# Kernel tuning notes

Hardware: AMD Instinct MI355X
Metric: run time of the kernel (lower is better)

The kernel has to match this reference:

```python
import jax, jax.numpy as jnp
import numpy as np

EPS = 1e-5
KH = KW = 3
PAD = 1

def conv3x3(x, w, b=None):
    out = jax.lax.conv_general_dilated(
        x, w, window_strides=(1, 1), padding=((PAD, PAD), (PAD, PAD)),
        dimension_numbers=("NCHW", "OIHW", "NCHW"))
    if b is not None:
        out = out + b[None, :, None, None]
    return out

def batchnorm(x, gamma, beta):
    # training-mode BatchNorm2d: batch statistics over (N, H, W)
    mean = x.mean(axis=(0, 2, 3), keepdims=True)
    var = x.var(axis=(0, 2, 3), keepdims=True)
    return gamma[None, :, None, None] * (x - mean) / jnp.sqrt(var + EPS) + beta[None, :, None, None]

def bilinear_gather(x, y_pos, x_pos):
    # x: [B,C,H,W]; y_pos/x_pos: [B,P,H,W] (P = KH*KW sampling taps)
    # zero padding outside image (mmcv modulated deform conv semantics)
    B, C, H, W = x.shape
    P = y_pos.shape[1]
    x_flat = x.reshape(B, C, H * W)
    y0 = jnp.floor(y_pos)
    x0 = jnp.floor(x_pos)
    ly = y_pos - y0
    lx = x_pos - x0
    out = jnp.zeros((B, C, P, H, W), dtype=x.dtype)
    for dy, dx, wgt in ((0, 0, (1 - ly) * (1 - lx)), (0, 1, (1 - ly) * lx),
                        (1, 0, ly * (1 - lx)), (1, 1, ly * lx)):
        yi = y0 + dy
        xi = x0 + dx
        valid = ((yi >= 0) & (yi <= H - 1) & (xi >= 0) & (xi <= W - 1)).astype(x.dtype)
        yc = jnp.clip(yi, 0, H - 1).astype(jnp.int32)
        xc = jnp.clip(xi, 0, W - 1).astype(jnp.int32)
        idx = (yc * W + xc).reshape(B, 1, P * H * W)
        vals = jnp.take_along_axis(x_flat, jnp.broadcast_to(idx, (B, C, P * H * W)), axis=2)
        vals = vals.reshape(B, C, P, H, W)
        out = out + vals * (wgt * valid)[:, None]
    return out  # [B,C,P,H,W]

def modulated_deform_conv(x, w_off, b_off, w_dcn):
    B, C, H, W = x.shape
    P = KH * KW
    off = conv3x3(x, w_off, b_off)  # [B, 3*P, H, W]
    o1, o2, m = jnp.split(off, 3, axis=1)
    offset = jnp.concatenate([o1, o2], axis=1)            # [B, 2P, H, W]
    offset = offset.reshape(B, P, 2, H, W)                # channel 2p -> dy, 2p+1 -> dx
    mask = jax.nn.sigmoid(m)                              # [B, P, H, W]
    hh = jnp.arange(H, dtype=x.dtype)
    ww = jnp.arange(W, dtype=x.dtype)
    ky = jnp.arange(KH, dtype=x.dtype)
    kx = jnp.arange(KW, dtype=x.dtype)
    # base sampling grid per tap p = ky*KW + kx: (h - PAD + ky, w - PAD + kx)
    base_y = (hh[None, :] - PAD + ky[:, None])            # [KH, H]
    base_x = (ww[None, :] - PAD + kx[:, None])            # [KW, W]
    base_y = jnp.broadcast_to(base_y[:, None, :, None], (KH, KW, H, W)).reshape(P, H, W)
    base_x = jnp.broadcast_to(base_x[None, :, None, :], (KH, KW, H, W)).reshape(P, H, W)
    y_pos = base_y[None] + offset[:, :, 0]                # [B,P,H,W]
    x_pos = base_x[None] + offset[:, :, 1]
    sampled = bilinear_gather(x, y_pos, x_pos)            # [B,C,P,H,W]
    sampled = sampled * mask[:, None]
    w = w_dcn.reshape(w_dcn.shape[0], C, P)               # [O, C, P]
    return jnp.einsum("bcphw,ocp->bohw", sampled, w)

def setup_inputs() -> dict:
    key = jax.random.key(0)
    ks = jax.random.split(key, 10)
    B, Ch, H, W = 4, 256, 64, 64
    Cin, Cout = 2 * Ch, 256
    P = KH * KW
    inp = {
        "input_v": jax.random.normal(ks[0], (B, Ch, H, W), jnp.float32),
        "input_i": jax.random.normal(ks[1], (B, Ch, H, W), jnp.float32),
        "w_off": jax.random.normal(ks[2], (3 * P, Cin, KH, KW), jnp.float32) * 0.01,
        "b_off": jnp.zeros((3 * P,), jnp.float32),
        "w_dcn": jax.random.normal(ks[3], (Cout, Cin, KH, KW), jnp.float32) * (1.0 / np.sqrt(Cin * P)),
        "gamma1": jnp.ones((Cout,), jnp.float32),
        "beta1": jnp.zeros((Cout,), jnp.float32),
        "w2": jax.random.normal(ks[4], (Cout, Cout, KH, KW), jnp.float32) * (1.0 / np.sqrt(Cout * P)),
        "gamma2": jnp.ones((Cout,), jnp.float32),
        "beta2": jnp.zeros((Cout,), jnp.float32),
    }
    return inp

def reference(input_v, input_i, w_off, b_off, w_dcn, gamma1, beta1, w2, gamma2, beta2):
    x = jnp.concatenate([input_v, input_i], axis=1)
    out = modulated_deform_conv(x, w_off, b_off, w_dcn)
    out = jax.nn.relu(batchnorm(out, gamma1, beta1))
    out = jax.nn.relu(batchnorm(conv3x3(out, w2), gamma2, beta2))
    return out
```

## Files before the change

### kernel.cpp

```cpp
#include <hip/hip_runtime.h>
#include <cstdint>
#include <cstddef>

typedef unsigned short u16;
typedef __attribute__((ext_vector_type(8))) short s16x8;
typedef __attribute__((ext_vector_type(4))) float f32x4;

#define DEV __device__ __forceinline__

DEV float bf2f(short u){
  union { unsigned int i; float f; } v;
  v.i = ((unsigned int)(u16)u) << 16;
  return v.f;
}
DEV short f2bf(float f){
  union { float f; unsigned int i; } v; v.f = f;
  unsigned int u = v.i;
  u += 0x7fffu + ((u >> 16) & 1u);
  return (short)(u >> 16);
}
DEV s16x8 s16x8_zero(){
  s16x8 z;
#pragma unroll
  for(int j=0;j<8;j++) z[j]=0;
  return z;
}
DEV f32x4 f32x4_zero(){
  f32x4 z;
#pragma unroll
  for(int j=0;j<4;j++) z[j]=0.f;
  return z;
}
DEV f32x4 mfma16(s16x8 a, s16x8 b, f32x4 c){
  return __builtin_amdgcn_mfma_f32_16x16x32_bf16(a, b, c, 0, 0, 0);
}

static constexpr size_t OFF_ACC_B  = 0;
static constexpr size_t OUT1_ACC_B = 2097152;
static constexpr size_t OUT2_ACC_B = OUT1_ACC_B + 16777216;
static constexpr size_t STATS_B    = OUT2_ACC_B + 16777216;
static constexpr size_t ZERO_BYTES = STATS_B + 4096;
static constexpr size_t XN_B       = ZERO_BYTES;
static constexpr size_t OUT1N_B    = XN_B + 16777216;
static constexpr size_t WOFFT_B    = OUT1N_B + 8388608;
static constexpr size_t WDCNT_B    = WOFFT_B + 294912;
static constexpr size_t W2T_B      = WDCNT_B + 2359296;

__global__ void k_x_to_nhwc(const float* __restrict__ v, const float* __restrict__ vi,
                            u16* __restrict__ xn){
  __shared__ float tile[64][65];
  const int b = blockIdx.z, c0 = blockIdx.y*64, hw0 = blockIdx.x*64;
  const float* src = (c0 < 256) ? (v  + ((size_t)b*256 + c0)      *4096)
                                : (vi + ((size_t)b*256 + (c0-256))*4096);
  const int t = threadIdx.x;
#pragma unroll
  for(int k=0;k<16;k++){
    int idx = t + k*256;
    int cl = idx >> 6, wl = idx & 63;
    tile[cl][wl] = src[(size_t)cl*4096 + hw0 + wl];
  }
  __syncthreads();
#pragma unroll
  for(int k=0;k<16;k++){
    int idx = t + k*256;
    int wl = idx >> 6, cl = idx & 63;
    xn[(size_t)(b*4096 + hw0 + wl)*512 + c0 + cl] = (u16)f2bf(tile[cl][wl]);
  }
}

__global__ void k_prep_woff(const float* __restrict__ w, u16* __restrict__ wt){
  int idx = blockIdx.x*256 + threadIdx.x;
  if(idx >= 32*4608) return;
  int n = idx / 4608, k = idx % 4608;
  int t = k >> 9, c = k & 511;
  float val = (n < 27) ? w[(size_t)(n*512 + c)*9 + t] : 0.f;
  wt[idx] = (u16)f2bf(val);
}
__global__ void k_prep_wdcn(const float* __restrict__ w, u16* __restrict__ wt){
  int idx = blockIdx.x*256 + threadIdx.x;
  if(idx >= 256*4608) return;
  int n = idx / 4608, k = idx % 4608;
  int t = k >> 9, c = k & 511;
  wt[idx] = (u16)f2bf(w[(size_t)(n*512 + c)*9 + t]);
}
__global__ void k_prep_w2(const float* __restrict__ w, u16* __restrict__ wt){
  int idx = blockIdx.x*256 + threadIdx.x;
  if(idx >= 256*2304) return;
  int n = idx / 2304, k = idx % 2304;
  int t = k >> 8, c = k & 255;
  wt[idx] = (u16)f2bf(w[(size_t)(n*256 + c)*9 + t]);
}

__global__ __launch_bounds__(256, 2) void k_conv_off(
    const u16* __restrict__ xn, const u16* __restrict__ wt, float* __restrict__ offa){
  __shared__ short A_lds[4][128][8];
  __shared__ short B_lds[4][32][8];
  const int tid = threadIdx.x;
  const int lane = tid & 63, wid = tid >> 6;
  const int quad = lane >> 4, ln = lane & 15;
  const int m0 = blockIdx.x * 128;
  const int b = m0 >> 12;
  const int h0 = (m0 & 4095) >> 6;
  const int ks = blockIdx.y;
  const int ts0 = (ks==0)?0:(ks==1)?2:(ks==2)?4:6;
  const int ts1 = (ks==0)?2:(ks==1)?4:(ks==2)?6:9;
  const int m_base = wid * 32;
  const int r = tid >> 1, sp = (tid & 1) * 2;
  const int h_r = h0 + (r >> 6), w_r = r & 63;
  const s16x8* Ap = (const s16x8*)A_lds;
  const s16x8* Bp = (const s16x8*)B_lds;
  f32x4 acc[2][2];
#pragma unroll
  for(int mf=0;mf<2;mf++)
#pragma unroll
    for(int nf=0;nf<2;nf++) acc[mf][nf] = f32x4_zero();

  for(int tp=ts0; tp<ts1; tp++){
    const int ty = tp/3, tx = tp - ty*3;
    const int y = h_r - 1 + ty, x = w_r - 1 + tx;
    const bool vld = (y>=0) & (y<64) & (x>=0) & (x<64);
    const u16* src = xn + (long)(b*4096 + y*64 + x)*512 + sp*8;
    const int kbase = tp*512;
    for(int cc=0; cc<16; cc++){
      const int c0 = cc*32;
      s16x8 v0 = s16x8_zero(), v1 = s16x8_zero();
      if(vld){
        v0 = *(const s16x8*)(src + c0);
        v1 = *(const s16x8*)(src + c0 + 8);
      }
      *(s16x8*)(&A_lds[sp][r][0])   = v0;
      *(s16x8*)(&A_lds[sp+1][r][0]) = v1;
      if(tid < 128){
        const int n = tid & 31, s2 = tid >> 5;
        *(s16x8*)(&B_lds[s2][n][0]) =
            *(const s16x8*)(wt + (size_t)n*4608 + kbase + c0 + s2*8);
      }
      __syncthreads();
      s16x8 a0 = Ap[quad*128 + m_base + ln];
      s16x8 a1 = Ap[quad*128 + m_base + 16 + ln];
      s16x8 b0 = Bp[quad*32 + ln];
      s16x8 b1 = Bp[quad*32 + 16 + ln];
      acc[0][0] = mfma16(a0, b0, acc[0][0]);
      acc[0][1] = mfma16(a0, b1, acc[0][1]);
      acc[1][0] = mfma16(a1, b0, acc[1][0]);
      acc[1][1] = mfma16(a1, b1, acc[1][1]);
      __syncthreads();
    }
  }
#pragma unroll
  for(int mf=0;mf<2;mf++)
#pragma unroll
    for(int nf=0;nf<2;nf++){
      const int col = nf*16 + ln;
#pragma unroll
      for(int i=0;i<4;i++){
        const int row = m_base + mf*16 + quad*4 + i;
        unsafeAtomicAdd(offa + (size_t)(m0+row)*32 + col, acc[mf][nf][i]);
      }
    }
}

__global__ __launch_bounds__(256, 2) void k_dcn(
    const u16* __restrict__ xn, const u16* __restrict__ wt,
    const float* __restrict__ offa, const float* __restrict__ boff,
    float* __restrict__ outa){
  __shared__ short A_lds[4][64][8];
  __shared__ short B_lds[4][256][8];
  __shared__ int   p_ofs[4][64];
  __shared__ float p_wgt[4][64];
  const int tid = threadIdx.x;
  const int lane = tid & 63, wid = tid >> 6;
  const int quad = lane >> 4, ln = lane & 15;
  const int m0 = blockIdx.x * 64;
  const int b = m0 >> 12;
  const int h = (m0 & 4095) >> 6;
  const int ts0 = blockIdx.y ? 4 : 0;
  const int ts1 = blockIdx.y ? 9 : 4;
  const int wm = wid >> 1, wn = wid & 1;
  const int m_base = wm*32, n_base = wn*128;
  const int r = tid >> 2, sub = tid & 3;
  const s16x8* Ap = (const s16x8*)A_lds;
  const s16x8* Bp = (const s16x8*)B_lds;
  f32x4 acc[2][8];
#pragma unroll
  for(int mf=0;mf<2;mf++)
#pragma unroll
    for(int nf=0;nf<8;nf++) acc[mf][nf] = f32x4_zero();

  for(int tp=ts0; tp<ts1; tp++){
    if(tid < 64){
      const int rr = tid;
      const float* orow = offa + (size_t)(m0+rr)*32;
      float dy = orow[2*tp]   + boff[2*tp];
      float dx = orow[2*tp+1] + boff[2*tp+1];
      float mz = orow[18+tp]  + boff[18+tp];
      float mk = 1.f / (1.f + expf(-mz));
      float ypos = (float)(h - 1 + tp/3) + dy;
      float xpos = (float)(rr - 1 + tp%3) + dx;
      float y0f = floorf(ypos), x0f = floorf(xpos);
      float ly = ypos - y0f, lx = xpos - x0f;
      int y0 = (int)y0f, x0 = (int)x0f;
#pragma unroll
      for(int k=0;k<4;k++){
        int ddy = k >> 1, ddx = k & 1;
        int yi = y0 + ddy, xi = x0 + ddx;
        bool vv = (yi >= 0) & (yi < 64) & (xi >= 0) & (xi < 64);
        float wk = (ddy ? ly : 1.f-ly) * (ddx ? lx : 1.f-lx) * mk;
        if(!vv) wk = 0.f;
        int yc = yi < 0 ? 0 : (yi > 63 ? 63 : yi);
        int xc = xi < 0 ? 0 : (xi > 63 ? 63 : xi);
        p_ofs[k][rr] = ((b << 12) + (yc << 6) + xc) << 9;
        p_wgt[k][rr] = wk;
      }
    }
    __syncthreads();
    const float w0f = p_wgt[0][r], w1f = p_wgt[1][r], w2f = p_wgt[2][r], w3f = p_wgt[3][r];
    const u16* s0p = xn + p_ofs[0][r] + sub*8;
    const u16* s1p = xn + p_ofs[1][r] + sub*8;
    const u16* s2p = xn + p_ofs[2][r] + sub*8;
    const u16* s3p = xn + p_ofs[3][r] + sub*8;
    const u16* wrow0 = wt + (size_t)tid*4608 + tp*512;

    for(int cc=0; cc<16; cc++){
      const int c0 = cc*32;
      s16x8 v0 = *(const s16x8*)(s0p + c0);
      s16x8 v1 = *(const s16x8*)(s1p + c0);
      s16x8 v2 = *(const s16x8*)(s2p + c0);
      s16x8 v3 = *(const s16x8*)(s3p + c0);
      s16x8 pk;
#pragma unroll
      for(int j=0;j<8;j++){
        float f = w0f * bf2f(v0[j]);
        f = fmaf(w1f, bf2f(v1[j]), f);
        f = fmaf(w2f, bf2f(v2[j]), f);
        f = fmaf(w3f, bf2f(v3[j]), f);
        pk[j] = f2bf(f);
      }
      *(s16x8*)(&A_lds[sub][r][0]) = pk;
#pragma unroll
      for(int s2=0; s2<4; s2++)
        *(s16x8*)(&B_lds[s2][tid][0]) = *(const s16x8*)(wrow0 + c0 + s2*8);
      __syncthreads();
      s16x8 af0 = Ap[quad*64 + m_base + ln];
      s16x8 af1 = Ap[quad*64 + m_base + 16 + ln];
      s16x8 bfr[8];
#pragma unroll
      for(int nf=0;nf<8;nf++) bfr[nf] = Bp[quad*256 + n_base + nf*16 + ln];
#pragma unroll
      for(int nf=0;nf<8;nf++){
        acc[0][nf] = mfma16(af0, bfr[nf], acc[0][nf]);
        acc[1][nf] = mfma16(af1, bfr[nf], acc[1][nf]);
      }
      __syncthreads();
    }
  }
#pragma unroll
  for(int mf=0;mf<2;mf++)
#pragma unroll
    for(int nf=0;nf<8;nf++){
      const int col = n_base + nf*16 + ln;
#pragma unroll
      for(int i=0;i<4;i++){
        const int row = m_base + mf*16 + quad*4 + i;
        unsafeAtomicAdd(outa + (size_t)(m0+row)*256 + col, acc[mf][nf][i]);
      }
    }
}

__global__ __launch_bounds__(256, 2) void k_conv2(
    const u16* __restrict__ a_in, const u16* __restrict__ wt, float* __restrict__ outa){
  __shared__ short A_lds[4][64][8];
  __shared__ short B_lds[4][256][8];
  const int tid = threadIdx.x;
  const int lane = tid & 63, wid = tid >> 6;
  const int quad = lane >> 4, ln = lane & 15;
  const int m0 = blockIdx.x * 64;
  const int b = m0 >> 12;
  const int h = (m0 & 4095) >> 6;
  const int ts0 = blockIdx.y ? 4 : 0;
  const int ts1 = blockIdx.y ? 9 : 4;
  const int wm = wid >> 1, wn = wid & 1;
  const int m_base = wm*32, n_base = wn*128;
  const int r = tid >> 2, sub = tid & 3;
  const s16x8* Ap = (const s16x8*)A_lds;
  const s16x8* Bp = (const s16x8*)B_lds;
  f32x4 acc[2][8];
#pragma unroll
  for(int mf=0;mf<2;mf++)
#pragma unroll
    for(int nf=0;nf<8;nf++) acc[mf][nf] = f32x4_zero();

  for(int tp=ts0; tp<ts1; tp++){
    const int ty = tp/3, tx = tp - ty*3;
    const int y = h - 1 + ty, x = r - 1 + tx;
    const bool vld = (y>=0) & (y<64) & (x>=0) & (x<64);
    const u16* src = a_in + (long)(b*4096 + y*64 + x)*256 + sub*8;
    const u16* wrow0 = wt + (size_t)tid*2304 + tp*256;
    for(int cc=0; cc<8; cc++){
      const int c0 = cc*32;
      s16x8 va = vld ? *(const s16x8*)(src + c0) : s16x8_zero();
      *(s16x8*)(&A_lds[sub][r][0]) = va;
#pragma unroll
      for(int s2=0;s2<4;s2++)
        *(s16x8*)(&B_lds[s2][tid][0]) = *(const s16x8*)(wrow0 + c0 + s2*8);
      __syncthreads();
      s16x8 af0 = Ap[quad*64 + m_base + ln];
      s16x8 af1 = Ap[quad*64 + m_base + 16 + ln];
      s16x8 bfr[8];
#pragma unroll
      for(int nf=0;nf<8;nf++) bfr[nf] = Bp[quad*256 + n_base + nf*16 + ln];
#pragma unroll
      for(int nf=0;nf<8;nf++){
        acc[0][nf] = mfma16(af0, bfr[nf], acc[0][nf]);
        acc[1][nf] = mfma16(af1, bfr[nf], acc[1][nf]);
      }
      __syncthreads();
    }
  }
#pragma unroll
  for(int mf=0;mf<2;mf++)
#pragma unroll
    for(int nf=0;nf<8;nf++){
      const int col = n_base + nf*16 + ln;
#pragma unroll
      for(int i=0;i<4;i++){
        const int row = m_base + mf*16 + quad*4 + i;
        unsafeAtomicAdd(outa + (size_t)(m0+row)*256 + col, acc[mf][nf][i]);
      }
    }
}

__global__ void k_stats(const float* __restrict__ acc, float* __restrict__ sum,
                        float* __restrict__ sq){
  const int m0 = blockIdx.x*64;
  const int c = threadIdx.x;
  float s = 0.f, q = 0.f;
  for(int i=0;i<64;i++){
    float v = acc[(size_t)(m0+i)*256 + c];
    s += v; q += v*v;
  }
  unsafeAtomicAdd(sum + c, s);
  unsafeAtomicAdd(sq + c, q);
}

__global__ void k_bn1(const float* __restrict__ acc, const float* __restrict__ sum,
                      const float* __restrict__ sq, const float* __restrict__ g,
                      const float* __restrict__ bt, u16* __restrict__ o){
  __shared__ float sc[256], sh[256];
  const int t = threadIdx.x;
  {
    float mean = sum[t] * (1.f/16384.f);
    float var  = sq[t] * (1.f/16384.f) - mean*mean;
    float rstd = rsqrtf(var + 1e-5f);
    float s = g[t] * rstd;
    sc[t] = s; sh[t] = bt[t] - mean*s;
  }
  __syncthreads();
  const int c4 = (t & 63) * 4;
  const float s0 = sc[c4], s1 = sc[c4+1], s2 = sc[c4+2], s3 = sc[c4+3];
  const float h0 = sh[c4], h1 = sh[c4+1], h2 = sh[c4+2], h3 = sh[c4+3];
#pragma unroll
  for(int k=0;k<4;k++){
    int m = blockIdx.x*16 + k*4 + (t>>6);
    const float4 v = *(const float4*)(acc + (size_t)m*256 + c4);
    unsigned int lo = (unsigned int)(u16)f2bf(fmaxf(0.f, v.x*s0 + h0))
                    | ((unsigned int)(u16)f2bf(fmaxf(0.f, v.y*s1 + h1)) << 16);
    unsigned int hi = (unsigned int)(u16)f2bf(fmaxf(0.f, v.z*s2 + h2))
                    | ((unsigned int)(u16)f2bf(fmaxf(0.f, v.w*s3 + h3)) << 16);
    uint2 pr; pr.x = lo; pr.y = hi;
    *(uint2*)(o + (size_t)m*256 + c4) = pr;
  }
}

__global__ void k_bn2_out(const float* __restrict__ acc, const float* __restrict__ sum,
                          const float* __restrict__ sq, const float* __restrict__ g,
                          const float* __restrict__ bt, float* __restrict__ out){
  __shared__ float tile[64][65];
  __shared__ float sc[64], sh[64];
  const int t = threadIdx.x;
  const int b = blockIdx.z, c0 = blockIdx.y*64, hw0 = blockIdx.x*64;
  if(t < 64){
    int c = c0 + t;
    float mean = sum[c] * (1.f/16384.f);
    float var  = sq[c] * (1.f/16384.f) - mean*mean;
    float rstd = rsqrtf(var + 1e-5f);
    float s = g[c] * rstd;
    sc[t] = s; sh[t] = bt[c] - mean*s;
  }
  __syncthreads();
#pragma unroll
  for(int k=0;k<16;k++){
    int idx = t + k*256;
    int wl = idx >> 6, cl = idx & 63;
    float v = acc[(size_t)((b<<12) + hw0 + wl)*256 + c0 + cl];
    tile[wl][cl] = fmaxf(0.f, v*sc[cl] + sh[cl]);
  }
  __syncthreads();
#pragma unroll
  for(int k=0;k<16;k++){
    int idx = t + k*256;
    int cl = idx >> 6, wl = idx & 63;
    out[(size_t)(b*256 + c0 + cl)*4096 + hw0 + wl] = tile[wl][cl];
  }
}

extern "C" void kernel_launch(void* const* d_in, const int* in_sizes, int n_in,
                              void* d_out, int out_size, void* d_ws, size_t ws_size,
                              hipStream_t stream){
  const float* in_v  = (const float*)d_in[0];
  const float* in_i  = (const float*)d_in[1];
  const float* w_off = (const float*)d_in[2];
  const float* b_off = (const float*)d_in[3];
  const float* w_dcn = (const float*)d_in[4];
  const float* g1    = (const float*)d_in[5];
  const float* bt1   = (const float*)d_in[6];
  const float* w2    = (const float*)d_in[7];
  const float* g2    = (const float*)d_in[8];
  const float* bt2   = (const float*)d_in[9];
  float* out = (float*)d_out;
  char* ws = (char*)d_ws;

  float* off_acc  = (float*)(ws + OFF_ACC_B);
  float* out1_acc = (float*)(ws + OUT1_ACC_B);
  float* out2_acc = (float*)(ws + OUT2_ACC_B);
  float* stats    = (float*)(ws + STATS_B);
  float* sum1 = stats,       *sq1 = stats + 256;
  float* sum2 = stats + 512, *sq2 = stats + 768;
  u16* xn    = (u16*)(ws + XN_B);
  u16* out1n = (u16*)(ws + OUT1N_B);
  u16* wofft = (u16*)(ws + WOFFT_B);
  u16* wdcnt = (u16*)(ws + WDCNT_B);
  u16* w2t   = (u16*)(ws + W2T_B);

  hipMemsetAsync(ws, 0, ZERO_BYTES, stream);
  k_x_to_nhwc<<<dim3(64,8,4), 256, 0, stream>>>(in_v, in_i, xn);
  k_prep_woff<<<576, 256, 0, stream>>>(w_off, wofft);
  k_prep_wdcn<<<4608, 256, 0, stream>>>(w_dcn, wdcnt);
  k_prep_w2<<<2304, 256, 0, stream>>>(w2, w2t);
  k_conv_off<<<dim3(128,4), 256, 0, stream>>>(xn, wofft, off_acc);
  k_dcn<<<dim3(256,2), 256, 0, stream>>>(xn, wdcnt, off_acc, b_off, out1_acc);
  k_stats<<<256, 256, 0, stream>>>(out1_acc, sum1, sq1);
  k_bn1<<<1024, 256, 0, stream>>>(out1_acc, sum1, sq1, g1, bt1, out1n);
  k_conv2<<<dim3(256,2), 256, 0, stream>>>(out1n, w2t, out2_acc);
  k_stats<<<256, 256, 0, stream>>>(out2_acc, sum2, sq2);
  k_bn2_out<<<dim3(64,4,4), 256, 0, stream>>>(out2_acc, sum2, sq2, g2, bt2, out);
}
```

Before: 378.1 us.

## Pad NHWC buffers, use direct global-to-LDS loads, precompute sampling, widen K steps

Stores the activations in zero-bordered padded NHWC buffers so the conv kernels can drop their bounds checks. Tiles now load straight into LDS with global_load_lds 16-byte copies, and each K-step doubles from 32 to 64 channels to halve the barriers. The bilinear sampling offsets and weights move into a separate k_sampler kernel that writes them to global memory. The tap split becomes 3 ways, with larger launch_bounds occupancy hints. This trades extra workspace, two additional kernel launches and a round trip of the sampling data through global memory for cheaper inner loops.

```diff
diff --git a/kernel.cpp b/kernel.cpp
--- a/kernel.cpp
+++ b/kernel.cpp
@@ -34,22 +34,40 @@
 DEV f32x4 mfma16(s16x8 a, s16x8 b, f32x4 c){
   return __builtin_amdgcn_mfma_f32_16x16x32_bf16(a, b, c, 0, 0, 0);
 }
-
-static constexpr size_t OFF_ACC_B  = 0;
-static constexpr size_t OUT1_ACC_B = 2097152;
-static constexpr size_t OUT2_ACC_B = OUT1_ACC_B + 16777216;
-static constexpr size_t STATS_B    = OUT2_ACC_B + 16777216;
-static constexpr size_t ZERO_BYTES = STATS_B + 4096;
-static constexpr size_t XN_B       = ZERO_BYTES;
-static constexpr size_t OUT1N_B    = XN_B + 16777216;
-static constexpr size_t WOFFT_B    = OUT1N_B + 8388608;
-static constexpr size_t WDCNT_B    = WOFFT_B + 294912;
-static constexpr size_t W2T_B      = WDCNT_B + 2359296;
+DEV void cp16(const void* g, void* l){
+  __builtin_amdgcn_global_load_lds(
+      (const __attribute__((address_space(1))) unsigned int*)g,
+      (__attribute__((address_space(3))) unsigned int*)l, 16, 0, 0);
+}
+
+static constexpr size_t OFF_ACC_B   = 0;
+static constexpr size_t OUT1_ACC_B  = 2097152;
+static constexpr size_t OUT2_ACC_B  = 18874368;
+static constexpr size_t STATS_B     = 35651584;
+static constexpr size_t ZERO_BYTES  = 35655680;
+static constexpr size_t XN_PAD_B    = 35655680;
+static constexpr size_t OUT1N_PAD_B = 53497856;
+static constexpr size_t WOFFT_B     = 62418944;
+static constexpr size_t WDCNT_B     = 62713856;
+static constexpr size_t W2T_B       = 65073152;
+static constexpr size_t SAMP_O_B    = 66252800;
+static constexpr size_t SAMP_W_B    = 68612096;
+
+__global__ void k_border(u16* __restrict__ xp, u16* __restrict__ op){
+  const int cid = blockIdx.x, t = threadIdx.x;
+  const int b = cid / 260, rem = cid % 260;
+  int y, x;
+  if(rem < 132){ y = (rem/66)*65; x = rem%66; }
+  else { int r2 = rem-132; x = (r2>>6)*65; y = 1 + (r2&63); }
+  const size_t cell = (size_t)(b*66+y)*66 + x;
+  ((unsigned int*)(xp + cell*512))[t] = 0;
+  if(t < 128) ((unsigned int*)(op + cell*256))[t] = 0;
+}
 
 __global__ void k_x_to_nhwc(const float* __restrict__ v, const float* __restrict__ vi,
                             u16* __restrict__ xn){
   __shared__ float tile[64][65];
-  const int b = blockIdx.z, c0 = blockIdx.y*64, hw0 = blockIdx.x*64;
+  const int b = blockIdx.z, c0 = blockIdx.y*64, h = blockIdx.x;
   const float* src = (c0 < 256) ? (v  + ((size_t)b*256 + c0)      *4096)
                                 : (vi + ((size_t)b*256 + (c0-256))*4096);
   const int t = threadIdx.x;
@@ -57,14 +75,14 @@
   for(int k=0;k<16;k++){
     int idx = t + k*256;
     int cl = idx >> 6, wl = idx & 63;
-    tile[cl][wl] = src[(size_t)cl*4096 + hw0 + wl];
+    tile[cl][wl] = src[(size_t)cl*4096 + h*64 + wl];
   }
   __syncthreads();
 #pragma unroll
   for(int k=0;k<16;k++){
     int idx = t + k*256;
     int wl = idx >> 6, cl = idx & 63;
-    xn[(size_t)(b*4096 + hw0 + wl)*512 + c0 + cl] = (u16)f2bf(tile[cl][wl]);
+    xn[((size_t)(b*66 + h+1)*66 + (wl+1))*512 + c0 + cl] = (u16)f2bf(tile[cl][wl]);
   }
 }
 
@@ -91,94 +109,101 @@
   wt[idx] = (u16)f2bf(w[(size_t)(n*256 + c)*9 + t]);
 }
 
-__global__ __launch_bounds__(256, 2) void k_conv_off(
+__global__ __launch_bounds__(256, 4) void k_conv_off(
     const u16* __restrict__ xn, const u16* __restrict__ wt, float* __restrict__ offa){
-  __shared__ short A_lds[4][128][8];
-  __shared__ short B_lds[4][32][8];
-  const int tid = threadIdx.x;
-  const int lane = tid & 63, wid = tid >> 6;
-  const int quad = lane >> 4, ln = lane & 15;
-  const int m0 = blockIdx.x * 128;
-  const int b = m0 >> 12;
-  const int h0 = (m0 & 4095) >> 6;
-  const int ks = blockIdx.y;
-  const int ts0 = (ks==0)?0:(ks==1)?2:(ks==2)?4:6;
-  const int ts1 = (ks==0)?2:(ks==1)?4:(ks==2)?6:9;
-  const int m_base = wid * 32;
-  const int r = tid >> 1, sp = (tid & 1) * 2;
-  const int h_r = h0 + (r >> 6), w_r = r & 63;
-  const s16x8* Ap = (const s16x8*)A_lds;
-  const s16x8* Bp = (const s16x8*)B_lds;
-  f32x4 acc[2][2];
-#pragma unroll
-  for(int mf=0;mf<2;mf++)
-#pragma unroll
-    for(int nf=0;nf<2;nf++) acc[mf][nf] = f32x4_zero();
-
-  for(int tp=ts0; tp<ts1; tp++){
-    const int ty = tp/3, tx = tp - ty*3;
-    const int y = h_r - 1 + ty, x = w_r - 1 + tx;
-    const bool vld = (y>=0) & (y<64) & (x>=0) & (x<64);
-    const u16* src = xn + (long)(b*4096 + y*64 + x)*512 + sp*8;
-    const int kbase = tp*512;
-    for(int cc=0; cc<16; cc++){
-      const int c0 = cc*32;
-      s16x8 v0 = s16x8_zero(), v1 = s16x8_zero();
-      if(vld){
-        v0 = *(const s16x8*)(src + c0);
-        v1 = *(const s16x8*)(src + c0 + 8);
-      }
-      *(s16x8*)(&A_lds[sp][r][0])   = v0;
-      *(s16x8*)(&A_lds[sp+1][r][0]) = v1;
-      if(tid < 128){
-        const int n = tid & 31, s2 = tid >> 5;
-        *(s16x8*)(&B_lds[s2][n][0]) =
-            *(const s16x8*)(wt + (size_t)n*4608 + kbase + c0 + s2*8);
-      }
-      __syncthreads();
-      s16x8 a0 = Ap[quad*128 + m_base + ln];
-      s16x8 a1 = Ap[quad*128 + m_base + 16 + ln];
-      s16x8 b0 = Bp[quad*32 + ln];
-      s16x8 b1 = Bp[quad*32 + 16 + ln];
-      acc[0][0] = mfma16(a0, b0, acc[0][0]);
-      acc[0][1] = mfma16(a0, b1, acc[0][1]);
-      acc[1][0] = mfma16(a1, b0, acc[1][0]);
-      acc[1][1] = mfma16(a1, b1, acc[1][1]);
-      __syncthreads();
-    }
-  }
-#pragma unroll
-  for(int mf=0;mf<2;mf++)
-#pragma unroll
-    for(int nf=0;nf<2;nf++){
-      const int col = nf*16 + ln;
-#pragma unroll
-      for(int i=0;i<4;i++){
-        const int row = m_base + mf*16 + quad*4 + i;
-        unsafeAtomicAdd(offa + (size_t)(m0+row)*32 + col, acc[mf][nf][i]);
-      }
-    }
-}
-
-__global__ __launch_bounds__(256, 2) void k_dcn(
-    const u16* __restrict__ xn, const u16* __restrict__ wt,
-    const float* __restrict__ offa, const float* __restrict__ boff,
-    float* __restrict__ outa){
-  __shared__ short A_lds[4][64][8];
-  __shared__ short B_lds[4][256][8];
-  __shared__ int   p_ofs[4][64];
-  __shared__ float p_wgt[4][64];
+  __shared__ short A_lds[8][64][8];
+  __shared__ short B_lds[8][32][8];
   const int tid = threadIdx.x;
   const int lane = tid & 63, wid = tid >> 6;
   const int quad = lane >> 4, ln = lane & 15;
   const int m0 = blockIdx.x * 64;
   const int b = m0 >> 12;
-  const int h = (m0 & 4095) >> 6;
-  const int ts0 = blockIdx.y ? 4 : 0;
-  const int ts1 = blockIdx.y ? 9 : 4;
-  const int wm = wid >> 1, wn = wid & 1;
-  const int m_base = wm*32, n_base = wn*128;
+  const int h = (m0 >> 6) & 63;
+  const int ks = blockIdx.y;
+  const int m_base = wid * 16;
+  const s16x8* Ap = (const s16x8*)A_lds;
+  const s16x8* Bp = (const s16x8*)B_lds;
+  f32x4 acc[2];
+  acc[0] = f32x4_zero(); acc[1] = f32x4_zero();
+
+  for(int tpi=0; tpi<3; tpi++){
+    const int tp = ks*3 + tpi;
+    const int ty = tp/3, tx = tp - ty*3;
+    const u16* arow = xn + ((size_t)(b*66 + h+ty)*66 + lane + tx)*512;
+    const u16* brow = wt + (size_t)(lane & 31)*4608 + tp*512 + (wid*2 + (lane>>5))*8;
+    for(int s=0; s<8; s++){
+      const int cb = s*64;
+      cp16(arow + cb + (wid*2)*8,     &A_lds[wid*2][0][0]);
+      cp16(arow + cb + (wid*2+1)*8,   &A_lds[wid*2+1][0][0]);
+      cp16(brow + cb,                 &B_lds[wid*2][0][0]);
+      __syncthreads();
+#pragma unroll
+      for(int cc=0; cc<2; cc++){
+        const int s2 = cc*4 + quad;
+        s16x8 a  = Ap[s2*64 + m_base + ln];
+        s16x8 b0 = Bp[s2*32 + ln];
+        s16x8 b1 = Bp[s2*32 + 16 + ln];
+        acc[0] = mfma16(a, b0, acc[0]);
+        acc[1] = mfma16(a, b1, acc[1]);
+      }
+      __syncthreads();
+    }
+  }
+#pragma unroll
+  for(int nf=0;nf<2;nf++){
+    const int col = nf*16 + ln;
+#pragma unroll
+    for(int i=0;i<4;i++){
+      const int row = m_base + quad*4 + i;
+      unsafeAtomicAdd(offa + (size_t)(m0+row)*32 + col, acc[nf][i]);
+    }
+  }
+}
+
+__global__ void k_sampler(const float* __restrict__ offa, const float* __restrict__ boff,
+                          int* __restrict__ so, float* __restrict__ sw){
+  const int idx = blockIdx.x*256 + threadIdx.x;
+  if(idx >= 16384*9) return;
+  const int m = idx / 9, tp = idx - m*9;
+  const int b = m >> 12, h = (m >> 6) & 63, w = m & 63;
+  const float* orow = offa + (size_t)m*32;
+  float dy = orow[2*tp]   + boff[2*tp];
+  float dx = orow[2*tp+1] + boff[2*tp+1];
+  float mz = orow[18+tp]  + boff[18+tp];
+  float mk = 1.f / (1.f + expf(-mz));
+  float ypos = (float)(h - 1 + tp/3) + dy;
+  float xpos = (float)(w - 1 + tp%3) + dx;
+  float y0f = floorf(ypos), x0f = floorf(xpos);
+  float ly = ypos - y0f, lx = xpos - x0f;
+  int y0 = (int)y0f, x0 = (int)x0f;
+#pragma unroll
+  for(int k=0;k<4;k++){
+    int ddy = k >> 1, ddx = k & 1;
+    int yi = y0 + ddy, xi = x0 + ddx;
+    bool vv = (yi >= 0) & (yi < 64) & (xi >= 0) & (xi < 64);
+    float wk = (ddy ? ly : 1.f-ly) * (ddx ? lx : 1.f-lx) * mk;
+    if(!vv) wk = 0.f;
+    int yc = yi < 0 ? 0 : (yi > 63 ? 63 : yi);
+    int xc = xi < 0 ? 0 : (xi > 63 ? 63 : xi);
+    so[(size_t)idx*4 + k] = ((b*66 + yc+1)*66 + xc+1) << 9;
+    sw[(size_t)idx*4 + k] = wk;
+  }
+}
+
+__global__ __launch_bounds__(256, 3) void k_dcn(
+    const u16* __restrict__ xn, const u16* __restrict__ wt,
+    const int* __restrict__ so, const float* __restrict__ sw,
+    float* __restrict__ outa){
+  __shared__ short A_lds[8][64][8];
+  __shared__ short B_lds[8][256][8];
+  const int tid = threadIdx.x;
+  const int lane = tid & 63, wid = tid >> 6;
+  const int quad = lane >> 4, ln = lane & 15;
+  const int m0 = blockIdx.x * 64;
+  const int ks = blockIdx.y;
+  const int m_base = (wid >> 1)*32, n_base = (wid & 1)*128;
   const int r = tid >> 2, sub = tid & 3;
+  const int nw = wid * 64;
   const s16x8* Ap = (const s16x8*)A_lds;
   const s16x8* Bp = (const s16x8*)B_lds;
   f32x4 acc[2][8];
@@ -187,69 +212,59 @@
 #pragma unroll
     for(int nf=0;nf<8;nf++) acc[mf][nf] = f32x4_zero();
 
-  for(int tp=ts0; tp<ts1; tp++){
-    if(tid < 64){
-      const int rr = tid;
-      const float* orow = offa + (size_t)(m0+rr)*32;
-      float dy = orow[2*tp]   + boff[2*tp];
-      float dx = orow[2*tp+1] + boff[2*tp+1];
-      float mz = orow[18+tp]  + boff[18+tp];
-      float mk = 1.f / (1.f + expf(-mz));
-      float ypos = (float)(h - 1 + tp/3) + dy;
-      float xpos = (float)(rr - 1 + tp%3) + dx;
-      float y0f = floorf(ypos), x0f = floorf(xpos);
-      float ly = ypos - y0f, lx = xpos - x0f;
-      int y0 = (int)y0f, x0 = (int)x0f;
-#pragma unroll
-      for(int k=0;k<4;k++){
-        int ddy = k >> 1, ddx = k & 1;
-        int yi = y0 + ddy, xi = x0 + ddx;
-        bool vv = (yi >= 0) & (yi < 64) & (xi >= 0) & (xi < 64);
-        float wk = (ddy ? ly : 1.f-ly) * (ddx ? lx : 1.f-lx) * mk;
-        if(!vv) wk = 0.f;
-        int yc = yi < 0 ? 0 : (yi > 63 ? 63 : yi);
-        int xc = xi < 0 ? 0 : (xi > 63 ? 63 : xi);
-        p_ofs[k][rr] = ((b << 12) + (yc << 6) + xc) << 9;
-        p_wgt[k][rr] = wk;
-      }
-    }
-    __syncthreads();
-    const float w0f = p_wgt[0][r], w1f = p_wgt[1][r], w2f = p_wgt[2][r], w3f = p_wgt[3][r];
-    const u16* s0p = xn + p_ofs[0][r] + sub*8;
-    const u16* s1p = xn + p_ofs[1][r] + sub*8;
-    const u16* s2p = xn + p_ofs[2][r] + sub*8;
-    const u16* s3p = xn + p_ofs[3][r] + sub*8;
-    const u16* wrow0 = wt + (size_t)tid*4608 + tp*512;
-
-    for(int cc=0; cc<16; cc++){
-      const int c0 = cc*32;
-      s16x8 v0 = *(const s16x8*)(s0p + c0);
-      s16x8 v1 = *(const s16x8*)(s1p + c0);
-      s16x8 v2 = *(const s16x8*)(s2p + c0);
-      s16x8 v3 = *(const s16x8*)(s3p + c0);
-      s16x8 pk;
+  for(int tpi=0; tpi<3; tpi++){
+    const int tp = ks*3 + tpi;
+    const int4   po = *(const int4*)  (so + ((size_t)(m0+r)*9 + tp)*4);
+    const float4 pw = *(const float4*)(sw + ((size_t)(m0+r)*9 + tp)*4);
+    const u16* a0p = xn + po.x + sub*8;
+    const u16* a1p = xn + po.y + sub*8;
+    const u16* a2p = xn + po.z + sub*8;
+    const u16* a3p = xn + po.w + sub*8;
+    const u16* bsrc = wt + (size_t)(nw + lane)*4608 + tp*512;
+
+    for(int s=0; s<8; s++){
+      const int c0 = s*64;
+      s16x8 v00 = *(const s16x8*)(a0p + c0);
+      s16x8 v01 = *(const s16x8*)(a1p + c0);
+      s16x8 v02 = *(const s16x8*)(a2p + c0);
+      s16x8 v03 = *(const s16x8*)(a3p + c0);
+      s16x8 v10 = *(const s16x8*)(a0p + c0 + 32);
+      s16x8 v11 = *(const s16x8*)(a1p + c0 + 32);
+      s16x8 v12 = *(const s16x8*)(a2p + c0 + 32);
+      s16x8 v13 = *(const s16x8*)(a3p + c0 + 32);
+#pragma unroll
+      for(int s2=0; s2<8; s2++)
+        cp16(bsrc + c0 + s2*8, &B_lds[s2][nw][0]);
+      s16x8 pk0, pk1;
 #pragma unroll
       for(int j=0;j<8;j++){
-        float f = w0f * bf2f(v0[j]);
-        f = fmaf(w1f, bf2f(v1[j]), f);
-        f = fmaf(w2f, bf2f(v2[j]), f);
-        f = fmaf(w3f, bf2f(v3[j]), f);
-        pk[j] = f2bf(f);
-      }
-      *(s16x8*)(&A_lds[sub][r][0]) = pk;
-#pragma unroll
-      for(int s2=0; s2<4; s2++)
-        *(s16x8*)(&B_lds[s2][tid][0]) = *(const s16x8*)(wrow0 + c0 + s2*8);
-      __syncthreads();
-      s16x8 af0 = Ap[quad*64 + m_base + ln];
-      s16x8 af1 = Ap[quad*64 + m_base + 16 + ln];
-      s16x8 bfr[8];
-#pragma unroll
-      for(int nf=0;nf<8;nf++) bfr[nf] = Bp[quad*256 + n_base + nf*16 + ln];
-#pragma unroll
-      for(int nf=0;nf<8;nf++){
-        acc[0][nf] = mfma16(af0, bfr[nf], acc[0][nf]);
-        acc[1][nf] = mfma16(af1, bfr[nf], acc[1][nf]);
+        float f0 = pw.x * bf2f(v00[j]);
+        f0 = fmaf(pw.y, bf2f(v01[j]), f0);
+        f0 = fmaf(pw.z, bf2f(v02[j]), f0);
+        f0 = fmaf(pw.w, bf2f(v03[j]), f0);
+        pk0[j] = f2bf(f0);
+        float f1 = pw.x * bf2f(v10[j]);
+        f1 = fmaf(pw.y, bf2f(v11[j]), f1);
+        f1 = fmaf(pw.z, bf2f(v12[j]), f1);
+        f1 = fmaf(pw.w, bf2f(v13[j]), f1);
+        pk1[j] = f2bf(f1);
+      }
+      *(s16x8*)(&A_lds[sub][r][0])     = pk0;
+      *(s16x8*)(&A_lds[sub+4][r][0])   = pk1;
+      __syncthreads();
+#pragma unroll
+      for(int cc=0; cc<2; cc++){
+        const int s2 = cc*4 + quad;
+        s16x8 a0 = Ap[s2*64 + m_base + ln];
+        s16x8 a1 = Ap[s2*64 + m_base + 16 + ln];
+        s16x8 bfr[8];
+#pragma unroll
+        for(int nf=0;nf<8;nf++) bfr[nf] = Bp[s2*256 + n_base + nf*16 + ln];
+#pragma unroll
+        for(int nf=0;nf<8;nf++){
+          acc[0][nf] = mfma16(a0, bfr[nf], acc[0][nf]);
+          acc[1][nf] = mfma16(a1, bfr[nf], acc[1][nf]);
+        }
       }
       __syncthreads();
     }
@@ -267,21 +282,19 @@
     }
 }
 
-__global__ __launch_bounds__(256, 2) void k_conv2(
+__global__ __launch_bounds__(256, 3) void k_conv2(
     const u16* __restrict__ a_in, const u16* __restrict__ wt, float* __restrict__ outa){
-  __shared__ short A_lds[4][64][8];
-  __shared__ short B_lds[4][256][8];
+  __shared__ short A_lds[8][64][8];
+  __shared__ short B_lds[8][256][8];
   const int tid = threadIdx.x;
   const int lane = tid & 63, wid = tid >> 6;
   const int quad = lane >> 4, ln = lane & 15;
   const int m0 = blockIdx.x * 64;
   const int b = m0 >> 12;
-  const int h = (m0 & 4095) >> 6;
-  const int ts0 = blockIdx.y ? 4 : 0;
-  const int ts1 = blockIdx.y ? 9 : 4;
-  const int wm = wid >> 1, wn = wid & 1;
-  const int m_base = wm*32, n_base = wn*128;
-  const int r = tid >> 2, sub = tid & 3;
+  const int h = (m0 >> 6) & 63;
+  const int ks = blockIdx.y;
+  const int m_base = (wid >> 1)*32, n_base = (wid & 1)*128;
+  const int nw = wid * 64;
   const s16x8* Ap = (const s16x8*)A_lds;
   const s16x8* Bp = (const s16x8*)B_lds;
   f32x4 acc[2][8];
@@ -290,29 +303,32 @@
 #pragma unroll
     for(int nf=0;nf<8;nf++) acc[mf][nf] = f32x4_zero();
 
-  for(int tp=ts0; tp<ts1; tp++){
+  for(int tpi=0; tpi<3; tpi++){
+    const int tp = ks*3 + tpi;
     const int ty = tp/3, tx = tp - ty*3;
-    const int y = h - 1 + ty, x = r - 1 + tx;
-    const bool vld = (y>=0) & (y<64) & (x>=0) & (x<64);
-    const u16* src = a_in + (long)(b*4096 + y*64 + x)*256 + sub*8;
-    const u16* wrow0 = wt + (size_t)tid*2304 + tp*256;
-    for(int cc=0; cc<8; cc++){
-      const int c0 = cc*32;
-      s16x8 va = vld ? *(const s16x8*)(src + c0) : s16x8_zero();
-      *(s16x8*)(&A_lds[sub][r][0]) = va;
-#pragma unroll
-      for(int s2=0;s2<4;s2++)
-        *(s16x8*)(&B_lds[s2][tid][0]) = *(const s16x8*)(wrow0 + c0 + s2*8);
-      __syncthreads();
-      s16x8 af0 = Ap[quad*64 + m_base + ln];
-      s16x8 af1 = Ap[quad*64 + m_base + 16 + ln];
-      s16x8 bfr[8];
-#pragma unroll
-      for(int nf=0;nf<8;nf++) bfr[nf] = Bp[quad*256 + n_base + nf*16 + ln];
-#pragma unroll
-      for(int nf=0;nf<8;nf++){
-        acc[0][nf] = mfma16(af0, bfr[nf], acc[0][nf]);
-        acc[1][nf] = mfma16(af1, bfr[nf], acc[1][nf]);
+    const u16* arow = a_in + ((size_t)(b*66 + h+ty)*66 + lane + tx)*256;
+    const u16* bsrc = wt + (size_t)(nw + lane)*2304 + tp*256;
+    for(int s=0; s<4; s++){
+      const int c0 = s*64;
+      cp16(arow + c0 + wid*8,       &A_lds[wid][0][0]);
+      cp16(arow + c0 + (wid+4)*8,   &A_lds[wid+4][0][0]);
+#pragma unroll
+      for(int s2=0; s2<8; s2++)
+        cp16(bsrc + c0 + s2*8, &B_lds[s2][nw][0]);
+      __syncthreads();
+#pragma unroll
+      for(int cc=0; cc<2; cc++){
+        const int s2 = cc*4 + quad;
+        s16x8 a0 = Ap[s2*64 + m_base + ln];
+        s16x8 a1 = Ap[s2*64 + m_base + 16 + ln];
+        s16x8 bfr[8];
+#pragma unroll
+        for(int nf=0;nf<8;nf++) bfr[nf] = Bp[s2*256 + n_base + nf*16 + ln];
+#pragma unroll
+        for(int nf=0;nf<8;nf++){
+          acc[0][nf] = mfma16(a0, bfr[nf], acc[0][nf]);
+          acc[1][nf] = mfma16(a1, bfr[nf], acc[1][nf]);
+        }
       }
       __syncthreads();
     }
@@ -362,13 +378,14 @@
 #pragma unroll
   for(int k=0;k<4;k++){
     int m = blockIdx.x*16 + k*4 + (t>>6);
+    int b = m >> 12, hh = (m >> 6) & 63, ww = m & 63;
     const float4 v = *(const float4*)(acc + (size_t)m*256 + c4);
     unsigned int lo = (unsigned int)(u16)f2bf(fmaxf(0.f, v.x*s0 + h0))
                     | ((unsigned int)(u16)f2bf(fmaxf(0.f, v.y*s1 + h1)) << 16);
     unsigned int hi = (unsigned int)(u16)f2bf(fmaxf(0.f, v.z*s2 + h2))
                     | ((unsigned int)(u16)f2bf(fmaxf(0.f, v.w*s3 + h3)) << 16);
     uint2 pr; pr.x = lo; pr.y = hi;
-    *(uint2*)(o + (size_t)m*256 + c4) = pr;
+    *(uint2*)(o + ((size_t)(b*66 + hh+1)*66 + ww+1)*256 + c4) = pr;
   }
 }
 
@@ -426,22 +443,26 @@
   float* stats    = (float*)(ws + STATS_B);
   float* sum1 = stats,       *sq1 = stats + 256;
   float* sum2 = stats + 512, *sq2 = stats + 768;
-  u16* xn    = (u16*)(ws + XN_B);
-  u16* out1n = (u16*)(ws + OUT1N_B);
+  u16* xn_pad    = (u16*)(ws + XN_PAD_B);
+  u16* out1n_pad = (u16*)(ws + OUT1N_PAD_B);
   u16* wofft = (u16*)(ws + WOFFT_B);
   u16* wdcnt = (u16*)(ws + WDCNT_B);
   u16* w2t   = (u16*)(ws + W2T_B);
+  int*   samp_o = (int*)(ws + SAMP_O_B);
+  float* samp_w = (float*)(ws + SAMP_W_B);
 
   hipMemsetAsync(ws, 0, ZERO_BYTES, stream);
-  k_x_to_nhwc<<<dim3(64,8,4), 256, 0, stream>>>(in_v, in_i, xn);
+  k_border<<<1040, 256, 0, stream>>>(xn_pad, out1n_pad);
+  k_x_to_nhwc<<<dim3(64,8,4), 256, 0, stream>>>(in_v, in_i, xn_pad);
   k_prep_woff<<<576, 256, 0, stream>>>(w_off, wofft);
   k_prep_wdcn<<<4608, 256, 0, stream>>>(w_dcn, wdcnt);
   k_prep_w2<<<2304, 256, 0, stream>>>(w2, w2t);
-  k_conv_off<<<dim3(128,4), 256, 0, stream>>>(xn, wofft, off_acc);
-  k_dcn<<<dim3(256,2), 256, 0, stream>>>(xn, wdcnt, off_acc, b_off, out1_acc);
+  k_conv_off<<<dim3(256,3), 256, 0, stream>>>(xn_pad, wofft, off_acc);
+  k_sampler<<<576, 256, 0, stream>>>(off_acc, b_off, samp_o, samp_w);
+  k_dcn<<<dim3(256,3), 256, 0, stream>>>(xn_pad, wdcnt, samp_o, samp_w, out1_acc);
   k_stats<<<256, 256, 0, stream>>>(out1_acc, sum1, sq1);
-  k_bn1<<<1024, 256, 0, stream>>>(out1_acc, sum1, sq1, g1, bt1, out1n);
-  k_conv2<<<dim3(256,2), 256, 0, stream>>>(out1n, w2t, out2_acc);
+  k_bn1<<<1024, 256, 0, stream>>>(out1_acc, sum1, sq1, g1, bt1, out1n_pad);
+  k_conv2<<<dim3(256,3), 256, 0, stream>>>(out1n_pad, w2t, out2_acc);
   k_stats<<<256, 256, 0, stream>>>(out2_acc, sum2, sq2);
   k_bn2_out<<<dim3(64,4,4), 256, 0, stream>>>(out2_acc, sum2, sq2, g2, bt2, out);
 }
```

Result: slower. 411.1 us (+8.7%).
